# Performance work log

Hardware: AMD Instinct MI355X
Metric: run time of the kernel (lower is better)

The kernel has to match this reference:

```python
import jax, jax.numpy as jnp
import numpy as np

NUM_CLASSES = 19  # number of distinct labels in targets (fill_max)


def setup_inputs() -> dict:
    key = jax.random.key(0)
    k1, k2 = jax.random.split(key)
    n, d = 262144, 128
    inputs = jax.random.normal(k1, (n, d), dtype=jnp.float32)
    targets = jax.random.randint(k2, (n,), 0, NUM_CLASSES, dtype=jnp.int64)
    return {"inputs": inputs, "targets": targets}


def reference(inputs, targets):
    # Same math as the O(n^2) torch loop: for each sample i, the center is the
    # mean of all samples sharing targets[i]. Computed as one segment-reduction
    # over labels followed by a gather.
    n = inputs.shape[0]
    sums = jax.ops.segment_sum(inputs, targets, num_segments=NUM_CLASSES)          # [C, d]
    counts = jax.ops.segment_sum(jnp.ones((n,), inputs.dtype), targets,
                                 num_segments=NUM_CLASSES)                          # [C]
    class_centers = sums / counts[:, None]                                          # [C, d]
    centers = class_centers[targets]                                                # [n, d]
    dist_pc = jnp.sqrt(jnp.sum((inputs - centers) ** 2, axis=1))                    # [n]
    return jnp.mean(dist_pc)
```

## Files before the change

### kernel.cpp

```cpp
#include <hip/hip_runtime.h>
#include <math.h>

#define NCLS 19
#define DIM  128
#define CD   (NCLS * DIM)
#define WPB  16

__device__ __forceinline__ void proc_pair(float* __restrict__ tbl,
                                          int* __restrict__ cnt,
                                          float4 v, int ca, int cb,
                                          int lane, int l31) {
    if (ca == cb) {
        v.x += __shfl_xor(v.x, 32, 64);
        v.y += __shfl_xor(v.y, 32, 64);
        v.z += __shfl_xor(v.z, 32, 64);
        v.w += __shfl_xor(v.w, 32, 64);
        float4* q = (float4*)&tbl[ca * DIM + l31 * 4];
        float4 a = *q;
        a.x += v.x; a.y += v.y; a.z += v.z; a.w += v.w;
        *q = a;
        if (lane == 0) cnt[ca] += 2;
    } else {
        int c = (lane >= 32) ? cb : ca;
        float4* q = (float4*)&tbl[c * DIM + l31 * 4];
        float4 a = *q;
        a.x += v.x; a.y += v.y; a.z += v.z; a.w += v.w;
        *q = a;
        if (lane == 0)  cnt[ca]++;
        if (lane == 32) cnt[cb]++;
    }
}

__global__ __launch_bounds__(1024) void k_accum(const float4* __restrict__ in4,
                                                const int* __restrict__ tgt,
                                                float* __restrict__ gsums,
                                                int* __restrict__ gcounts,
                                                int npair) {
    __shared__ __align__(16) float ls[WPB * CD];
    __shared__ int lcnt[WPB * NCLS];
    const int tid  = threadIdx.x;
    const int w    = tid >> 6;
    const int lane = tid & 63;
    const int l31  = lane & 31;
    float* tbl = &ls[w * CD];
    int*   cnt = &lcnt[w * NCLS];

    for (int i = tid; i < WPB * CD; i += 1024) ls[i] = 0.0f;
    for (int i = tid; i < WPB * NCLS; i += 1024) lcnt[i] = 0;
    __syncthreads();

    const int stride = gridDim.x * WPB;
    int p = blockIdx.x * WPB + w;

    for (; p + 3 * stride < npair; p += 4 * stride) {
        float4 v0 = in4[(size_t)(p             ) * 64 + lane];
        float4 v1 = in4[(size_t)(p +     stride) * 64 + lane];
        float4 v2 = in4[(size_t)(p + 2 * stride) * 64 + lane];
        float4 v3 = in4[(size_t)(p + 3 * stride) * 64 + lane];
        int a0 = tgt[2 * p];                 int b0 = tgt[2 * p + 1];
        int a1 = tgt[2 * (p + stride)];      int b1 = tgt[2 * (p + stride) + 1];
        int a2 = tgt[2 * (p + 2 * stride)];  int b2 = tgt[2 * (p + 2 * stride) + 1];
        int a3 = tgt[2 * (p + 3 * stride)];  int b3 = tgt[2 * (p + 3 * stride) + 1];
        proc_pair(tbl, cnt, v0, a0, b0, lane, l31);
        proc_pair(tbl, cnt, v1, a1, b1, lane, l31);
        proc_pair(tbl, cnt, v2, a2, b2, lane, l31);
        proc_pair(tbl, cnt, v3, a3, b3, lane, l31);
    }
    for (; p < npair; p += stride) {
        float4 v = in4[(size_t)p * 64 + lane];
        int ca = tgt[2 * p];
        int cb = tgt[2 * p + 1];
        proc_pair(tbl, cnt, v, ca, cb, lane, l31);
    }
    __syncthreads();

    for (int i = tid; i < CD; i += 1024) {
        float s = 0.0f;
        #pragma unroll
        for (int ww = 0; ww < WPB; ww++) s += ls[ww * CD + i];
        unsafeAtomicAdd(&gsums[i], s);
    }
    if (tid < NCLS) {
        int s = 0;
        #pragma unroll
        for (int ww = 0; ww < WPB; ww++) s += lcnt[ww * NCLS + tid];
        atomicAdd(&gcounts[tid], s);
    }
}

__global__ __launch_bounds__(256) void k_dist(const float4* __restrict__ in4,
                                              const int* __restrict__ tgt,
                                              const float* __restrict__ gsums,
                                              const int* __restrict__ gcounts,
                                              float* __restrict__ out,
                                              int n, float inv_n) {
    __shared__ __align__(16) float lcent[CD];
    __shared__ float red[256];
    const int tid = threadIdx.x;

    for (int i = tid; i < CD; i += 256)
        lcent[i] = gsums[i] / (float)gcounts[i >> 7];
    __syncthreads();

    const int l32 = tid & 31;
    const int g   = tid >> 5;
    const int stride = gridDim.x * 8;
    float acc = 0.0f;
    int row = blockIdx.x * 8 + g;

    for (; row + stride < n; row += 2 * stride) {
        float4 va = in4[(size_t)row * 32 + l32];
        float4 vb = in4[(size_t)(row + stride) * 32 + l32];
        int ca = tgt[row];
        int cb = tgt[row + stride];
        float4 ea = *(const float4*)&lcent[ca * DIM + l32 * 4];
        float4 eb = *(const float4*)&lcent[cb * DIM + l32 * 4];
        float dx, dy, dz, dw;
        dx = va.x - ea.x; dy = va.y - ea.y; dz = va.z - ea.z; dw = va.w - ea.w;
        float d0 = dx * dx + dy * dy + dz * dz + dw * dw;
        dx = vb.x - eb.x; dy = vb.y - eb.y; dz = vb.z - eb.z; dw = vb.w - eb.w;
        float d1 = dx * dx + dy * dy + dz * dz + dw * dw;
        for (int off = 16; off > 0; off >>= 1) {
            d0 += __shfl_down(d0, off, 32);
            d1 += __shfl_down(d1, off, 32);
        }
        if (l32 == 0) acc += sqrtf(d0) + sqrtf(d1);
    }
    for (; row < n; row += stride) {
        float4 v = in4[(size_t)row * 32 + l32];
        int c = tgt[row];
        float4 ce = *(const float4*)&lcent[c * DIM + l32 * 4];
        float dx = v.x - ce.x, dy = v.y - ce.y, dz = v.z - ce.z, dw = v.w - ce.w;
        float d2 = dx * dx + dy * dy + dz * dz + dw * dw;
        for (int off = 16; off > 0; off >>= 1)
            d2 += __shfl_down(d2, off, 32);
        if (l32 == 0) acc += sqrtf(d2);
    }

    red[tid] = acc;
    __syncthreads();
    for (int s = 128; s > 0; s >>= 1) {
        if (tid < s) red[tid] += red[tid + s];
        __syncthreads();
    }
    if (tid == 0) unsafeAtomicAdd(out, red[0] * inv_n);
}

extern "C" void kernel_launch(void* const* d_in, const int* in_sizes, int n_in,
                              void* d_out, int out_size, void* d_ws, size_t ws_size,
                              hipStream_t stream) {
    const float* in  = (const float*)d_in[0];
    const int*   tgt = (const int*)d_in[1];
    const int n = in_sizes[0] / DIM;

    float* gsums   = (float*)d_ws;
    int*   gcounts = (int*)(gsums + CD);
    float* out     = (float*)d_out;

    hipMemsetAsync(d_ws, 0, CD * sizeof(float) + NCLS * sizeof(int), stream);
    hipMemsetAsync(d_out, 0, sizeof(float), stream);

    k_accum<<<256, 1024, 0, stream>>>((const float4*)in, tgt, gsums, gcounts,
                                      n / 2);
    k_dist<<<1024, 256, 0, stream>>>((const float4*)in, tgt, gsums, gcounts,
                                     out, n, 1.0f / (float)n);
}
```

Before: 231.8 us.

## Use contiguous per-block segments with staged targets and block-wide count histogram

Both kernels switch from grid-strided row assignment to contiguous per-block segments. Each block stages its slice of targets in shared memory. Counts come from a single shared-memory atomic histogram instead of per-warp counters inside the pair loop. Unroll depth rises to 8 loads in accumulation and 4 rows in distance. The code assumes n divides evenly into blocks and that each block covers exactly 1024 targets (256 in dist); for other shapes it would silently miss or misread rows.

```diff
diff --git a/kernel.cpp b/kernel.cpp
--- a/kernel.cpp
+++ b/kernel.cpp
@@ -7,7 +7,6 @@
 #define WPB  16
 
 __device__ __forceinline__ void proc_pair(float* __restrict__ tbl,
-                                          int* __restrict__ cnt,
                                           float4 v, int ca, int cb,
                                           int lane, int l31) {
     if (ca == cb) {
@@ -19,15 +18,12 @@
         float4 a = *q;
         a.x += v.x; a.y += v.y; a.z += v.z; a.w += v.w;
         *q = a;
-        if (lane == 0) cnt[ca] += 2;
     } else {
         int c = (lane >= 32) ? cb : ca;
         float4* q = (float4*)&tbl[c * DIM + l31 * 4];
         float4 a = *q;
         a.x += v.x; a.y += v.y; a.z += v.z; a.w += v.w;
         *q = a;
-        if (lane == 0)  cnt[ca]++;
-        if (lane == 32) cnt[cb]++;
     }
 }
 
@@ -37,55 +33,54 @@
                                                 int* __restrict__ gcounts,
                                                 int npair) {
     __shared__ __align__(16) float ls[WPB * CD];
-    __shared__ int lcnt[WPB * NCLS];
+    __shared__ int ltgt[1024];
+    __shared__ int lcnt[NCLS];
     const int tid  = threadIdx.x;
     const int w    = tid >> 6;
     const int lane = tid & 63;
     const int l31  = lane & 31;
     float* tbl = &ls[w * CD];
-    int*   cnt = &lcnt[w * NCLS];
+
+    const int ppb  = npair / gridDim.x;
+    const int pseg = blockIdx.x * ppb;
 
     for (int i = tid; i < WPB * CD; i += 1024) ls[i] = 0.0f;
-    for (int i = tid; i < WPB * NCLS; i += 1024) lcnt[i] = 0;
+    if (tid < NCLS) lcnt[tid] = 0;
+    ltgt[tid] = tgt[2 * pseg + tid];
     __syncthreads();
 
-    const int stride = gridDim.x * WPB;
-    int p = blockIdx.x * WPB + w;
+    atomicAdd(&lcnt[ltgt[tid]], 1);
 
-    for (; p + 3 * stride < npair; p += 4 * stride) {
-        float4 v0 = in4[(size_t)(p             ) * 64 + lane];
-        float4 v1 = in4[(size_t)(p +     stride) * 64 + lane];
-        float4 v2 = in4[(size_t)(p + 2 * stride) * 64 + lane];
-        float4 v3 = in4[(size_t)(p + 3 * stride) * 64 + lane];
-        int a0 = tgt[2 * p];                 int b0 = tgt[2 * p + 1];
-        int a1 = tgt[2 * (p + stride)];      int b1 = tgt[2 * (p + stride) + 1];
-        int a2 = tgt[2 * (p + 2 * stride)];  int b2 = tgt[2 * (p + 2 * stride) + 1];
-        int a3 = tgt[2 * (p + 3 * stride)];  int b3 = tgt[2 * (p + 3 * stride) + 1];
-        proc_pair(tbl, cnt, v0, a0, b0, lane, l31);
-        proc_pair(tbl, cnt, v1, a1, b1, lane, l31);
-        proc_pair(tbl, cnt, v2, a2, b2, lane, l31);
-        proc_pair(tbl, cnt, v3, a3, b3, lane, l31);
+    const int iters = ppb / WPB;
+    int i = 0;
+    for (; i + 7 < iters; i += 8) {
+        float4 v[8];
+        int ca[8], cb[8];
+        #pragma unroll
+        for (int j = 0; j < 8; j++) {
+            int pl = w + (i + j) * WPB;
+            v[j] = in4[(size_t)(pseg + pl) * 64 + lane];
+            ca[j] = ltgt[2 * pl];
+            cb[j] = ltgt[2 * pl + 1];
+        }
+        #pragma unroll
+        for (int j = 0; j < 8; j++)
+            proc_pair(tbl, v[j], ca[j], cb[j], lane, l31);
     }
-    for (; p < npair; p += stride) {
-        float4 v = in4[(size_t)p * 64 + lane];
-        int ca = tgt[2 * p];
-        int cb = tgt[2 * p + 1];
-        proc_pair(tbl, cnt, v, ca, cb, lane, l31);
+    for (; i < iters; i++) {
+        int pl = w + i * WPB;
+        float4 v = in4[(size_t)(pseg + pl) * 64 + lane];
+        proc_pair(tbl, v, ltgt[2 * pl], ltgt[2 * pl + 1], lane, l31);
     }
     __syncthreads();
 
-    for (int i = tid; i < CD; i += 1024) {
+    for (int k = tid; k < CD; k += 1024) {
         float s = 0.0f;
         #pragma unroll
-        for (int ww = 0; ww < WPB; ww++) s += ls[ww * CD + i];
-        unsafeAtomicAdd(&gsums[i], s);
+        for (int ww = 0; ww < WPB; ww++) s += ls[ww * CD + k];
+        unsafeAtomicAdd(&gsums[k], s);
     }
-    if (tid < NCLS) {
-        int s = 0;
-        #pragma unroll
-        for (int ww = 0; ww < WPB; ww++) s += lcnt[ww * NCLS + tid];
-        atomicAdd(&gcounts[tid], s);
-    }
+    if (tid < NCLS) atomicAdd(&gcounts[tid], lcnt[tid]);
 }
 
 __global__ __launch_bounds__(256) void k_dist(const float4* __restrict__ in4,
@@ -96,40 +91,48 @@
                                               int n, float inv_n) {
     __shared__ __align__(16) float lcent[CD];
     __shared__ float red[256];
+    __shared__ int ltgt[256];
     const int tid = threadIdx.x;
+
+    const int rpb  = n / gridDim.x;
+    const int rseg = blockIdx.x * rpb;
 
     for (int i = tid; i < CD; i += 256)
         lcent[i] = gsums[i] / (float)gcounts[i >> 7];
+    ltgt[tid] = tgt[rseg + tid];
     __syncthreads();
 
     const int l32 = tid & 31;
     const int g   = tid >> 5;
-    const int stride = gridDim.x * 8;
+    const int sub = rpb / 8;
     float acc = 0.0f;
-    int row = blockIdx.x * 8 + g;
 
-    for (; row + stride < n; row += 2 * stride) {
-        float4 va = in4[(size_t)row * 32 + l32];
-        float4 vb = in4[(size_t)(row + stride) * 32 + l32];
-        int ca = tgt[row];
-        int cb = tgt[row + stride];
-        float4 ea = *(const float4*)&lcent[ca * DIM + l32 * 4];
-        float4 eb = *(const float4*)&lcent[cb * DIM + l32 * 4];
-        float dx, dy, dz, dw;
-        dx = va.x - ea.x; dy = va.y - ea.y; dz = va.z - ea.z; dw = va.w - ea.w;
-        float d0 = dx * dx + dy * dy + dz * dz + dw * dw;
-        dx = vb.x - eb.x; dy = vb.y - eb.y; dz = vb.z - eb.z; dw = vb.w - eb.w;
-        float d1 = dx * dx + dy * dy + dz * dz + dw * dw;
-        for (int off = 16; off > 0; off >>= 1) {
-            d0 += __shfl_down(d0, off, 32);
-            d1 += __shfl_down(d1, off, 32);
+    int r = 0;
+    for (; r + 3 < sub; r += 4) {
+        float4 v[4], e[4];
+        #pragma unroll
+        for (int j = 0; j < 4; j++) {
+            int rl = g * sub + r + j;
+            v[j] = in4[(size_t)(rseg + rl) * 32 + l32];
+            e[j] = *(const float4*)&lcent[ltgt[rl] * DIM + l32 * 4];
         }
-        if (l32 == 0) acc += sqrtf(d0) + sqrtf(d1);
+        float d[4];
+        #pragma unroll
+        for (int j = 0; j < 4; j++) {
+            float dx = v[j].x - e[j].x, dy = v[j].y - e[j].y;
+            float dz = v[j].z - e[j].z, dw = v[j].w - e[j].w;
+            d[j] = dx * dx + dy * dy + dz * dz + dw * dw;
+        }
+        #pragma unroll
+        for (int j = 0; j < 4; j++)
+            for (int off = 16; off > 0; off >>= 1)
+                d[j] += __shfl_down(d[j], off, 32);
+        if (l32 == 0) acc += sqrtf(d[0]) + sqrtf(d[1]) + sqrtf(d[2]) + sqrtf(d[3]);
     }
-    for (; row < n; row += stride) {
-        float4 v = in4[(size_t)row * 32 + l32];
-        int c = tgt[row];
-        float4 ce = *(const float4*)&lcent[c * DIM + l32 * 4];
+    for (; r < sub; r++) {
+        int rl = g * sub + r;
+        float4 v = in4[(size_t)(rseg + rl) * 32 + l32];
+        float4 ce = *(const float4*)&lcent[ltgt[rl] * DIM + l32 * 4];
         float dx = v.x - ce.x, dy = v.y - ce.y, dz = v.z - ce.z, dw = v.w - ce.w;
         float d2 = dx * dx + dy * dy + dz * dz + dw * dw;
         for (int off = 16; off > 0; off >>= 1)
```

New measurement: 233.7 us. About the same (+0.8%).
